# Optimization experiments

Hardware: AMD Instinct MI355X
Metric: run time of the kernel (lower is better)

Reference implementation:

```python
import jax, jax.numpy as jnp
import numpy as np

PC_RANGE = (-51.2, -51.2, -5.0, 51.2, 51.2, 3.0)
NUM_HEADS = 8
K_TOKENS = 512
DS = 4  # bev_downsample


def _ln(x, w, b):
    m = x.mean(-1, keepdims=True)
    v = ((x - m) ** 2).mean(-1, keepdims=True)
    return (x - m) * jax.lax.rsqrt(v + 1e-5) * w + b


def _mlp(x, w1, b1, w2, b2):
    return jnp.maximum(x @ w1.T + b1, 0.0) @ w2.T + b2


def setup_inputs() -> dict:
    key = jax.random.key(0)
    ks = jax.random.split(key, 16)
    B, N, Dq, Dkv, H, W = 2, 1220, 512, 256, 512, 512
    s = 0.02
    rn = lambda k, shp: jax.random.normal(k, shp, jnp.float32) * s
    inp = {
        'instance_feature': jax.random.normal(ks[0], (B, N, Dq), jnp.float32),
        'pts_feats': jax.random.normal(ks[1], (B, Dkv, H, W), jnp.float32),
        'anchor': jax.random.normal(ks[2], (B, N, 11), jnp.float32) * 20.0,
        # cross-attention (kdim=vdim=256, embed_dim=512)
        'qw': rn(ks[3], (Dq, Dq)), 'qb': jnp.zeros((Dq,), jnp.float32),
        'kw': rn(ks[4], (Dq, Dkv)), 'kb': jnp.zeros((Dq,), jnp.float32),
        'vw': rn(ks[5], (Dq, Dkv)), 'vb': jnp.zeros((Dq,), jnp.float32),
        'aow': rn(ks[6], (Dq, Dq)), 'aob': jnp.zeros((Dq,), jnp.float32),
        # layer norms
        'qn_w': jnp.ones((Dq,), jnp.float32), 'qn_b': jnp.zeros((Dq,), jnp.float32),
        'tn_w': jnp.ones((Dkv,), jnp.float32), 'tn_b': jnp.zeros((Dkv,), jnp.float32),
        'on_w': jnp.ones((Dq,), jnp.float32), 'on_b': jnp.zeros((Dq,), jnp.float32),
        # out_proj
        'opw': rn(ks[7], (Dq, Dq)), 'opb': jnp.zeros((Dq,), jnp.float32),
        # bev_pos_mlp: Linear(2,256) -> ReLU -> Linear(256,256)
        'bp_w1': rn(ks[8], (Dkv, 2)), 'bp_b1': jnp.zeros((Dkv,), jnp.float32),
        'bp_w2': rn(ks[9], (Dkv, Dkv)), 'bp_b2': jnp.zeros((Dkv,), jnp.float32),
        # anchor_pos_mlp: Linear(2,512) -> ReLU -> Linear(512,512)
        'ap_w1': rn(ks[10], (Dq, 2)), 'ap_b1': jnp.zeros((Dq,), jnp.float32),
        'ap_w2': rn(ks[11], (Dq, Dq)), 'ap_b2': jnp.zeros((Dq,), jnp.float32),
        # gate: Linear(512,512) -> ReLU -> Linear(512,512) -> Sigmoid, bias init -2.0
        'g_w1': rn(ks[12], (Dq, Dq)), 'g_b1': jnp.zeros((Dq,), jnp.float32),
        'g_w2': rn(ks[13], (Dq, Dq)), 'g_b2': jnp.full((Dq,), -2.0, jnp.float32),
    }
    return inp


def reference(instance_feature, pts_feats, anchor,
              qw, qb, kw, kb, vw, vb, aow, aob,
              qn_w, qn_b, tn_w, tn_b, on_w, on_b,
              opw, opb,
              bp_w1, bp_b1, bp_w2, bp_b2,
              ap_w1, ap_b1, ap_w2, ap_b2,
              g_w1, g_b1, g_w2, g_b2):
    B, C, H0, W0 = pts_feats.shape
    # avg_pool2d(kernel=stride=DS)
    H, W = H0 // DS, W0 // DS
    bev = pts_feats.reshape(B, C, H, DS, W, DS).mean(axis=(3, 5))  # [B,C,H,W]
    # topk token selection by mean squared activation
    score = (bev ** 2).mean(axis=1).reshape(B, H * W)
    K = min(K_TOKENS, H * W)
    _, idx = jax.lax.top_k(score, K)  # [B,K], sorted descending
    tokens = bev.reshape(B, C, H * W).transpose(0, 2, 1)  # [B,HW,C]
    lidar_tokens = jnp.take_along_axis(tokens, idx[..., None], axis=1)  # [B,K,C]
    ys = idx // W
    xs = idx % W
    token_pos = jnp.stack([(xs.astype(jnp.float32) + 0.5) / W,
                           (ys.astype(jnp.float32) + 0.5) / H], axis=-1)  # [B,K,2]
    lidar_tokens = lidar_tokens + _mlp(token_pos, bp_w1, bp_b1, bp_w2, bp_b2)
    # anchor positional prior (anchor detached in original)
    xr = (anchor[..., 0] - PC_RANGE[0]) / (PC_RANGE[3] - PC_RANGE[0])
    yr = (anchor[..., 1] - PC_RANGE[1]) / (PC_RANGE[4] - PC_RANGE[1])
    xy = jnp.clip(jnp.stack([xr, yr], axis=-1), 0.0, 1.0)
    query_input = instance_feature + _mlp(xy, ap_w1, ap_b1, ap_w2, ap_b2)
    query = _ln(query_input, qn_w, qn_b)
    kv = _ln(lidar_tokens, tn_w, tn_b)
    # multihead cross-attention (dropout off / eval mode)
    Dq = query.shape[-1]
    hd = Dq // NUM_HEADS
    q = (query @ qw.T + qb).reshape(B, -1, NUM_HEADS, hd)  # [B,N,h,d]
    k = (kv @ kw.T + kb).reshape(B, K, NUM_HEADS, hd)      # [B,K,h,d]
    v = (kv @ vw.T + vb).reshape(B, K, NUM_HEADS, hd)
    scale = 1.0 / jnp.sqrt(jnp.float32(hd))
    att = jax.nn.softmax(jnp.einsum('bnhd,bkhd->bhnk', q, k) * scale, axis=-1)
    ctx = jnp.einsum('bhnk,bkhd->bnhd', att, v).reshape(B, -1, Dq)
    ctx = ctx @ aow.T + aob  # MHA out_proj
    lidar_context = _ln(ctx @ opw.T + opb, on_w, on_b)
    gate = jax.nn.sigmoid(_mlp(query_input, g_w1, g_b1, g_w2, g_b2))
    return instance_feature + gate * lidar_context
```

## Files before the change

### kernel.cpp

```cpp
#include <hip/hip_runtime.h>
#include <hip/hip_bf16.h>
#include <math.h>

constexpr int BB  = 2;
constexpr int NN  = 1220;
constexpr int DKV = 256;
constexpr int H0  = 512, W0 = 512;
constexpr int HH  = 128, WW = 128;
constexpr int HW  = HH * WW;
constexpr int KT  = 512;
constexpr int MR  = BB * NN;

typedef __attribute__((ext_vector_type(8)))  short bf16x8;
typedef __attribute__((ext_vector_type(4)))  float f32x4;
typedef __attribute__((ext_vector_type(16))) float f32x16;

constexpr size_t B_BEV   = 0;
constexpr size_t B_SCORE = 33554432;
constexpr size_t B_IDX   = 33685504;
constexpr size_t B_WBF   = 33689600;
constexpr size_t B_KV    = 37359616;
constexpr size_t B_KG    = 37883904;
constexpr size_t B_VG    = 38932480;
constexpr size_t B_VT    = 39981056;
constexpr size_t B_H1    = 41029632;
constexpr size_t B_QI32  = 43651072;
constexpr size_t B_QI16  = 48893952;
constexpr size_t B_QUERY = 51515392;
constexpr size_t B_QG    = 54136832;
constexpr size_t B_CTX   = 56758272;
constexpr size_t B_AO    = 59379712;
constexpr size_t B_OPO   = 62001152;
constexpr size_t B_LC    = 67244032;
constexpr size_t B_G1    = 72486912;
constexpr size_t WS_NEED = 75112448;

constexpr size_t WO_QW = 0, WO_KW = 262144, WO_VW = 393216, WO_AOW = 524288,
                 WO_OPW = 786432, WO_APW2 = 1048576, WO_GW1 = 1310720, WO_GW2 = 1572864;

__device__ __forceinline__ void gload_lds16(void* lds, const void* g) {
  __builtin_amdgcn_global_load_lds((const __attribute__((address_space(1))) unsigned int*)g,
                                   (__attribute__((address_space(3))) unsigned int*)lds, 16, 0, 0);
}

__device__ __forceinline__ unsigned cvt_pk_bf16(float a, float b) {
  unsigned r;
  asm("v_cvt_pk_bf16_f32 %0, %1, %2" : "=v"(r) : "v"(a), "v"(b));
  return r;
}

__global__ __launch_bounds__(256) void wconv_kernel(
    const float* __restrict__ qw, const float* __restrict__ kw,
    const float* __restrict__ vw, const float* __restrict__ aow,
    const float* __restrict__ opw, const float* __restrict__ apw2,
    const float* __restrict__ gw1, const float* __restrict__ gw2,
    __hip_bfloat16* __restrict__ dst) {
  int i = blockIdx.x * 256 + threadIdx.x;
  const float* src; int off;
  if (i < 262144)       { src = qw;   off = 0; }
  else if (i < 393216)  { src = kw;   off = 262144; }
  else if (i < 524288)  { src = vw;   off = 393216; }
  else if (i < 786432)  { src = aow;  off = 524288; }
  else if (i < 1048576) { src = opw;  off = 786432; }
  else if (i < 1310720) { src = apw2; off = 1048576; }
  else if (i < 1572864) { src = gw1;  off = 1310720; }
  else                  { src = gw2;  off = 1572864; }
  dst[i] = __float2bfloat16(src[i - off]);
}

__global__ __launch_bounds__(256) void poolscore_kernel(const float* __restrict__ pts,
    float* __restrict__ bev, float* __restrict__ score) {
  int g = blockIdx.x * 256 + threadIdx.x;
  int b = g >> 14;
  int p = g & (HW - 1);
  int h = p >> 7, w = p & (WW - 1);
  const float* base = pts + (((size_t)(b * 256) * 512) + h * 4) * 512 + w * 4;
  float acc = 0.f;
#pragma unroll 4
  for (int c = 0; c < 256; ++c) {
    const float* pc = base + (size_t)c * 262144;
    float s = 0.f;
#pragma unroll
    for (int r = 0; r < 4; ++r) {
      float4 v = *(const float4*)(pc + r * W0);
      s += v.x + v.y + v.z + v.w;
    }
    float sv = s * (1.f / 16.f);
    bev[((size_t)(b * 256 + c) << 14) + p] = sv;
    acc += sv * sv;
  }
  score[g] = acc * (1.f / 256.f);
}

__global__ __launch_bounds__(1024) void topk_kernel(const float* __restrict__ score,
                                                    int* __restrict__ idx) {
  int b = blockIdx.x;
  const float* s = score + b * HW;
  __shared__ int hist[16][256];
  __shared__ int htot[256];
  __shared__ int pscan[1024];
  __shared__ int sh_digit, sh_need, sh_cnt;
  int tid = threadIdx.x;
  int wv = tid >> 6;
  unsigned prefix = 0;
  int need = KT;
  for (int pass = 0; pass < 4; ++pass) {
    int shift = 24 - pass * 8;
    if (tid < 256) {
#pragma unroll
      for (int w = 0; w < 16; ++w) hist[w][tid] = 0;
    }
    __syncthreads();
    for (int p = tid; p < HW; p += 1024) {
      unsigned u = __float_as_uint(s[p]);
      bool match = (pass == 0) || ((u >> (shift + 8)) == prefix);
      if (match) atomicAdd(&hist[wv][(u >> shift) & 255], 1);
    }
    __syncthreads();
    if (tid < 256) {
      int t = 0;
#pragma unroll
      for (int w = 0; w < 16; ++w) t += hist[w][tid];
      htot[tid] = t;
    }
    __syncthreads();
    for (int off = 1; off < 256; off <<= 1) {
      int v = 0;
      if (tid < 256) v = htot[tid] + ((tid + off < 256) ? htot[tid + off] : 0);
      __syncthreads();
      if (tid < 256) htot[tid] = v;
      __syncthreads();
    }
    if (tid < 256) {
      int sfx = htot[tid], sfx1 = (tid < 255) ? htot[tid + 1] : 0;
      if (sfx >= need && sfx1 < need) { sh_digit = tid; sh_need = need - sfx1; }
    }
    __syncthreads();
    prefix = (prefix << 8) | (unsigned)sh_digit;
    need = sh_need;
    __syncthreads();
  }
  unsigned T = prefix;
  int r = need;
  if (tid == 0) sh_cnt = 0;
  __syncthreads();
  for (int p = tid; p < HW; p += 1024) {
    if (__float_as_uint(s[p]) > T) {
      int pos = atomicAdd(&sh_cnt, 1);
      idx[b * KT + pos] = p;
    }
  }
  __syncthreads();
  int base = sh_cnt;
  int base0 = tid * 16;
  int cnt = 0;
#pragma unroll
  for (int j = 0; j < 16; ++j) cnt += (__float_as_uint(s[base0 + j]) == T);
  pscan[tid] = cnt;
  __syncthreads();
  for (int off = 1; off < 1024; off <<= 1) {
    int v = pscan[tid];
    int add = (tid >= off) ? pscan[tid - off] : 0;
    __syncthreads();
    pscan[tid] = v + add;
    __syncthreads();
  }
  int rank = pscan[tid] - cnt;
  for (int j = 0; j < 16 && rank < r; ++j) {
    int p = base0 + j;
    if (__float_as_uint(s[p]) == T) {
      idx[b * KT + base + rank] = p;
      ++rank;
    }
  }
}

__global__ __launch_bounds__(256) void token_kernel(const float* __restrict__ bev,
    const int* __restrict__ idx,
    const float* __restrict__ bw1, const float* __restrict__ bb1,
    const float* __restrict__ bw2, const float* __restrict__ bb2,
    const float* __restrict__ tw, const float* __restrict__ tb,
    __hip_bfloat16* __restrict__ kv) {
  int blk = blockIdx.x;
  int b = blk >> 9;
  int c = threadIdx.x;
  int p = idx[blk];
  float val = bev[((size_t)(b * DKV + c) << 14) + p];
  float px = ((p & (WW - 1)) + 0.5f) * (1.f / WW);
  float py = ((p >> 7) + 0.5f) * (1.f / HH);
  __shared__ float h1[DKV];
  __shared__ float red[DKV];
  h1[c] = fmaxf(bw1[c * 2] * px + bw1[c * 2 + 1] * py + bb1[c], 0.f);
  __syncthreads();
  float o = bb2[c];
  const float4* w4 = (const float4*)(bw2 + c * DKV);
#pragma unroll 4
  for (int j = 0; j < DKV / 4; ++j) {
    float4 w = w4[j];
    o += w.x * h1[j * 4] + w.y * h1[j * 4 + 1] + w.z * h1[j * 4 + 2] + w.w * h1[j * 4 + 3];
  }
  float tokv = val + o;
  red[c] = tokv; __syncthreads();
  for (int st = 128; st > 0; st >>= 1) { if (c < st) red[c] += red[c + st]; __syncthreads(); }
  float mean = red[0] * (1.f / DKV);
  __syncthreads();
  float d = tokv - mean;
  red[c] = d * d; __syncthreads();
  for (int st = 128; st > 0; st >>= 1) { if (c < st) red[c] += red[c + st]; __syncthreads(); }
  float inv = rsqrtf(red[0] * (1.f / DKV) + 1e-5f);
  kv[(size_t)blk * DKV + c] = __float2bfloat16(d * inv * tw[c] + tb[c]);
}

__global__ __launch_bounds__(256) void ap1_kernel(const float* __restrict__ anchor,
    const float* __restrict__ w1, const float* __restrict__ b1,
    __hip_bfloat16* __restrict__ h) {
  int g = blockIdx.x * 256 + threadIdx.x;
  int row = g >> 9, col = g & 511;
  float ax = anchor[row * 11 + 0];
  float ay = anchor[row * 11 + 1];
  float xr = fminf(fmaxf((ax + 51.2f) * (1.f / 102.4f), 0.f), 1.f);
  float yr = fminf(fmaxf((ay + 51.2f) * (1.f / 102.4f), 0.f), 1.f);
  h[g] = __float2bfloat16(fmaxf(w1[col * 2] * xr + w1[col * 2 + 1] * yr + b1[col], 0.f));
}

template <int EPI>
__global__ __launch_bounds__(256) void mgemm(
    const short* __restrict__ A, const short* __restrict__ W,
    const float* __restrict__ bias, const float* __restrict__ aux1,
    const float* __restrict__ aux2, void* __restrict__ o1, void* __restrict__ o2,
    int M, int Nd, int Kd) {
  __shared__ short As[2][64 * 64];
  __shared__ short Bs[2][64 * 64];
  const int tid = threadIdx.x;
  const int wave = tid >> 6, lane = tid & 63;
  const int m0 = blockIdx.y * 64, n0 = blockIdx.x * 64;
  const int wr = wave >> 1, wc = wave & 1;
  const int srow = lane >> 3, sslot = lane & 7;
  const int ss = sslot ^ srow;
  f32x4 acc[2][2];
#pragma unroll
  for (int i = 0; i < 2; ++i)
#pragma unroll
    for (int j = 0; j < 2; ++j) acc[i][j] = (f32x4){0.f, 0.f, 0.f, 0.f};

  const short* Abase = A + (size_t)(m0 + srow) * Kd + ss * 8;
  const short* Wbase = W + (size_t)(n0 + srow) * Kd + ss * 8;
  const int nk = Kd >> 6;

#define STAGE(buf, k0)                                                        \
  {                                                                           \
    _Pragma("unroll")                                                         \
    for (int u = 0; u < 2; ++u) {                                             \
      int unit = wave * 2 + u;                                                \
      gload_lds16(&As[buf][unit * 512], Abase + (size_t)(unit * 8) * Kd + (k0)); \
      gload_lds16(&Bs[buf][unit * 512], Wbase + (size_t)(unit * 8) * Kd + (k0)); \
    }                                                                         \
  }

  STAGE(0, 0);
  __syncthreads();
  for (int t = 0; t < nk; ++t) {
    if (t + 1 < nk) STAGE((t + 1) & 1, (t + 1) << 6);
    const short* as = As[t & 1];
    const short* bs = Bs[t & 1];
#pragma unroll
    for (int ks = 0; ks < 2; ++ks) {
      bf16x8 af[2], bf[2];
#pragma unroll
      for (int mf = 0; mf < 2; ++mf) {
        int rr = wr * 32 + mf * 16 + (lane & 15);
        int slot = (ks * 4 + (lane >> 4)) ^ (rr & 7);
        af[mf] = *(const bf16x8*)(as + rr * 64 + slot * 8);
      }
#pragma unroll
      for (int nf = 0; nf < 2; ++nf) {
        int rr = wc * 32 + nf * 16 + (lane & 15);
        int slot = (ks * 4 + (lane >> 4)) ^ (rr & 7);
        bf[nf] = *(const bf16x8*)(bs + rr * 64 + slot * 8);
      }
#pragma unroll
      for (int mf = 0; mf < 2; ++mf)
#pragma unroll
        for (int nf = 0; nf < 2; ++nf)
          acc[mf][nf] = __builtin_amdgcn_mfma_f32_16x16x32_bf16(af[mf], bf[nf], acc[mf][nf], 0, 0, 0);
    }
    __syncthreads();
  }
#undef STAGE
#pragma unroll
  for (int mf = 0; mf < 2; ++mf)
#pragma unroll
    for (int nf = 0; nf < 2; ++nf) {
      int col = n0 + wc * 32 + nf * 16 + (lane & 15);
      float bv = bias[col];
#pragma unroll
      for (int i = 0; i < 4; ++i) {
        int row = m0 + wr * 32 + mf * 16 + (lane >> 4) * 4 + i;
        if (row < M) {
          float v = acc[mf][nf][i] + bv;
          size_t off = (size_t)row * Nd + col;
          if (EPI == 0) ((__hip_bfloat16*)o1)[off] = __float2bfloat16(v);
          else if (EPI == 1) {
            v += aux1[off];
            ((float*)o1)[off] = v;
            ((__hip_bfloat16*)o2)[off] = __float2bfloat16(v);
          } else if (EPI == 2) ((__hip_bfloat16*)o1)[off] = __float2bfloat16(fmaxf(v, 0.f));
          else if (EPI == 3) ((__hip_bfloat16*)o1)[off] = __float2bfloat16(v * 0.125f);
          else if (EPI == 4) ((float*)o1)[off] = v;
          else if (EPI == 5) {
            float g = 1.f / (1.f + __expf(-v));
            ((float*)o1)[off] = aux1[off] + g * aux2[off];
          }
        }
      }
    }
}

template <int OUT_BF16>
__global__ __launch_bounds__(256) void ln512_kernel(const float* __restrict__ in,
    void* __restrict__ outp, const float* __restrict__ w, const float* __restrict__ bb) {
  int row = blockIdx.x, tid = threadIdx.x;
  float x0 = in[(size_t)row * 512 + tid];
  float x1 = in[(size_t)row * 512 + 256 + tid];
  __shared__ float rs[256], rq[256];
  rs[tid] = x0 + x1;
  rq[tid] = x0 * x0 + x1 * x1;
  __syncthreads();
  for (int o = 128; o > 0; o >>= 1) {
    if (tid < o) { rs[tid] += rs[tid + o]; rq[tid] += rq[tid + o]; }
    __syncthreads();
  }
  float mean = rs[0] * (1.f / 512.f);
  float var = rq[0] * (1.f / 512.f) - mean * mean;
  float inv = rsqrtf(var + 1e-5f);
  float y0 = (x0 - mean) * inv * w[tid] + bb[tid];
  float y1 = (x1 - mean) * inv * w[256 + tid] + bb[256 + tid];
  if (OUT_BF16) {
    ((__hip_bfloat16*)outp)[(size_t)row * 512 + tid] = __float2bfloat16(y0);
    ((__hip_bfloat16*)outp)[(size_t)row * 512 + 256 + tid] = __float2bfloat16(y1);
  } else {
    ((float*)outp)[(size_t)row * 512 + tid] = y0;
    ((float*)outp)[(size_t)row * 512 + 256 + tid] = y1;
  }
}

__global__ __launch_bounds__(256) void vtrans_kernel(const short* __restrict__ V,
                                                     short* __restrict__ Vt) {
  __shared__ short tile[128][72];
  int tc = blockIdx.x, h = blockIdx.y, b = blockIdx.z;
  int tid = threadIdx.x;
#pragma unroll
  for (int it = 0; it < 8; ++it) {
    int e = it * 256 + tid;
    int r = e >> 4, c = (e & 15) * 4;
    *(short4*)&tile[r][c] =
        *(const short4*)(V + ((size_t)(b * 512 + tc * 128 + r)) * 512 + h * 64 + c);
  }
  __syncthreads();
#pragma unroll
  for (int it = 0; it < 8; ++it) {
    int e = it * 256 + tid;
    int d = e >> 5, t4 = (e & 31) * 4;
    short4 v;
    v.x = tile[t4 + 0][d]; v.y = tile[t4 + 1][d];
    v.z = tile[t4 + 2][d]; v.w = tile[t4 + 3][d];
    *(short4*)(Vt + (((size_t)(b * 8 + h)) * 64 + d) * 512 + tc * 128 + t4) = v;
  }
}

__global__ __launch_bounds__(256) void attn_kernel(
    const short* __restrict__ Qg, const short* __restrict__ Kg,
    const short* __restrict__ Vt, __hip_bfloat16* __restrict__ ctx) {
  int tid = threadIdx.x;
  int wid = blockIdx.x * 4 + (tid >> 6);
  int lane = tid & 63;
  int l31 = lane & 31, lhi = lane >> 5;
  int qc = wid % 39;
  int bh = wid / 39;
  int h = bh & 7, b = bh >> 3;
  int n = qc * 32 + l31;
  size_t qrow = (size_t)b * NN + n;
  const short* qp = Qg + qrow * 512 + h * 64 + lhi * 8;
  bf16x8 qf0 = *(const bf16x8*)(qp);
  bf16x8 qf1 = *(const bf16x8*)(qp + 16);
  bf16x8 qf2 = *(const bf16x8*)(qp + 32);
  bf16x8 qf3 = *(const bf16x8*)(qp + 48);
  f32x16 ot0 = {}, ot1 = {};
  float m_run = -1e30f, lsum = 0.f;
  const short* kbase = Kg + ((size_t)(b * KT) + l31) * 512 + h * 64 + lhi * 8;
  const short* vbase = Vt + (((size_t)(b * 8 + h)) * 64 + l31) * 512 + lhi * 8;
  for (int tc = 0; tc < 16; ++tc) {
    const short* kp = kbase + (size_t)(tc * 32) * 512;
    bf16x8 kf0 = *(const bf16x8*)(kp);
    bf16x8 kf1 = *(const bf16x8*)(kp + 16);
    bf16x8 kf2 = *(const bf16x8*)(kp + 32);
    bf16x8 kf3 = *(const bf16x8*)(kp + 48);
    const short* vp = vbase + tc * 32;
    bf16x8 v00 = *(const bf16x8*)(vp);
    bf16x8 v01 = *(const bf16x8*)(vp + 16);
    bf16x8 v10 = *(const bf16x8*)(vp + 32 * 512);
    bf16x8 v11 = *(const bf16x8*)(vp + 32 * 512 + 16);
    f32x16 s = {};
    s = __builtin_amdgcn_mfma_f32_32x32x16_bf16(kf0, qf0, s, 0, 0, 0);
    s = __builtin_amdgcn_mfma_f32_32x32x16_bf16(kf1, qf1, s, 0, 0, 0);
    s = __builtin_amdgcn_mfma_f32_32x32x16_bf16(kf2, qf2, s, 0, 0, 0);
    s = __builtin_amdgcn_mfma_f32_32x32x16_bf16(kf3, qf3, s, 0, 0, 0);
    float pmax = s[0];
#pragma unroll
    for (int i = 1; i < 16; ++i) pmax = fmaxf(pmax, s[i]);
    pmax = fmaxf(pmax, __shfl_xor(pmax, 32));
    float m_new = fmaxf(m_run, pmax);
    float corr = __expf(m_run - m_new);
    m_run = m_new;
    lsum *= corr;
#pragma unroll
    for (int i = 0; i < 16; ++i) { ot0[i] *= corr; ot1[i] *= corr; }
    float p[16];
    float psum = 0.f;
#pragma unroll
    for (int i = 0; i < 16; ++i) { p[i] = __expf(s[i] - m_new); psum += p[i]; }
    lsum += psum;
    unsigned w0 = cvt_pk_bf16(p[0], p[1]),   w1 = cvt_pk_bf16(p[2], p[3]);
    unsigned w2 = cvt_pk_bf16(p[4], p[5]),   w3 = cvt_pk_bf16(p[6], p[7]);
    unsigned w4 = cvt_pk_bf16(p[8], p[9]),   w5 = cvt_pk_bf16(p[10], p[11]);
    unsigned w6 = cvt_pk_bf16(p[12], p[13]), w7 = cvt_pk_bf16(p[14], p[15]);
    unsigned sw0 = (unsigned)__shfl_xor((int)w0, 32), sw1 = (unsigned)__shfl_xor((int)w1, 32);
    unsigned sw2 = (unsigned)__shfl_xor((int)w2, 32), sw3 = (unsigned)__shfl_xor((int)w3, 32);
    unsigned sw4 = (unsigned)__shfl_xor((int)w4, 32), sw5 = (unsigned)__shfl_xor((int)w5, 32);
    unsigned sw6 = (unsigned)__shfl_xor((int)w6, 32), sw7 = (unsigned)__shfl_xor((int)w7, 32);
    union UU { unsigned u[4]; bf16x8 v; };
    UU ub0, ub1;
    ub0.u[0] = lhi ? sw2 : w0; ub0.u[1] = lhi ? sw3 : w1;
    ub0.u[2] = lhi ? w2 : sw0; ub0.u[3] = lhi ? w3 : sw1;
    ub1.u[0] = lhi ? sw6 : w4; ub1.u[1] = lhi ? sw7 : w5;
    ub1.u[2] = lhi ? w6 : sw4; ub1.u[3] = lhi ? w7 : sw5;
    ot0 = __builtin_amdgcn_mfma_f32_32x32x16_bf16(v00, ub0.v, ot0, 0, 0, 0);
    ot0 = __builtin_amdgcn_mfma_f32_32x32x16_bf16(v01, ub1.v, ot0, 0, 0, 0);
    ot1 = __builtin_amdgcn_mfma_f32_32x32x16_bf16(v10, ub0.v, ot1, 0, 0, 0);
    ot1 = __builtin_amdgcn_mfma_f32_32x32x16_bf16(v11, ub1.v, ot1, 0, 0, 0);
  }
  lsum += __shfl_xor(lsum, 32);
  float inv = 1.f / lsum;
  if (n < NN) {
    __hip_bfloat16* cp = ctx + qrow * 512 + h * 64;
#pragma unroll
    for (int r = 0; r < 16; ++r) {
      int d = (r & 3) + 8 * (r >> 2) + 4 * lhi;
      cp[d]      = __float2bfloat16(ot0[r] * inv);
      cp[32 + d] = __float2bfloat16(ot1[r] * inv);
    }
  }
}

extern "C" void kernel_launch(void* const* d_in, const int* in_sizes, int n_in,
                              void* d_out, int out_size, void* d_ws, size_t ws_size,
                              hipStream_t stream) {
  const float* inst   = (const float*)d_in[0];
  const float* pts    = (const float*)d_in[1];
  const float* anchor = (const float*)d_in[2];
  const float* qw  = (const float*)d_in[3];
  const float* qb  = (const float*)d_in[4];
  const float* kw  = (const float*)d_in[5];
  const float* kb  = (const float*)d_in[6];
  const float* vw  = (const float*)d_in[7];
  const float* vb  = (const float*)d_in[8];
  const float* aow = (const float*)d_in[9];
  const float* aob = (const float*)d_in[10];
  const float* qnw = (const float*)d_in[11];
  const float* qnb = (const float*)d_in[12];
  const float* tnw = (const float*)d_in[13];
  const float* tnb = (const float*)d_in[14];
  const float* onw = (const float*)d_in[15];
  const float* onb = (const float*)d_in[16];
  const float* opw = (const float*)d_in[17];
  const float* opb = (const float*)d_in[18];
  const float* bpw1 = (const float*)d_in[19];
  const float* bpb1 = (const float*)d_in[20];
  const float* bpw2 = (const float*)d_in[21];
  const float* bpb2 = (const float*)d_in[22];
  const float* apw1 = (const float*)d_in[23];
  const float* apb1 = (const float*)d_in[24];
  const float* apw2 = (const float*)d_in[25];
  const float* apb2 = (const float*)d_in[26];
  const float* gw1 = (const float*)d_in[27];
  const float* gb1 = (const float*)d_in[28];
  const float* gw2 = (const float*)d_in[29];
  const float* gb2 = (const float*)d_in[30];
  float* out = (float*)d_out;

  if (ws_size < WS_NEED) return;
  char* ws = (char*)d_ws;
  float* bev   = (float*)(ws + B_BEV);
  float* score = (float*)(ws + B_SCORE);
  int*   idx   = (int*)(ws + B_IDX);
  short* wbf   = (short*)(ws + B_WBF);
  __hip_bfloat16* kvb = (__hip_bfloat16*)(ws + B_KV);
  short* Kgb  = (short*)(ws + B_KG);
  short* Vgb  = (short*)(ws + B_VG);
  short* Vtb  = (short*)(ws + B_VT);
  short* h1b  = (short*)(ws + B_H1);
  float* qi32 = (float*)(ws + B_QI32);
  short* qi16 = (short*)(ws + B_QI16);
  short* qryb = (short*)(ws + B_QUERY);
  short* Qgb  = (short*)(ws + B_QG);
  short* ctxb = (short*)(ws + B_CTX);
  short* aobuf = (short*)(ws + B_AO);
  float* opo  = (float*)(ws + B_OPO);
  float* lc   = (float*)(ws + B_LC);
  short* g1b  = (short*)(ws + B_G1);

  wconv_kernel<<<7168, 256, 0, stream>>>(qw, kw, vw, aow, opw, apw2, gw1, gw2,
                                         (__hip_bfloat16*)wbf);
  poolscore_kernel<<<BB * HW / 256, 256, 0, stream>>>(pts, bev, score);
  topk_kernel<<<BB, 1024, 0, stream>>>(score, idx);
  token_kernel<<<BB * KT, 256, 0, stream>>>(bev, idx, bpw1, bpb1, bpw2, bpb2, tnw, tnb, kvb);
  mgemm<0><<<dim3(8, 16), 256, 0, stream>>>((const short*)kvb, wbf + WO_KW, kb,
                                            nullptr, nullptr, Kgb, nullptr, 1024, 512, 256);
  mgemm<0><<<dim3(8, 16), 256, 0, stream>>>((const short*)kvb, wbf + WO_VW, vb,
                                            nullptr, nullptr, Vgb, nullptr, 1024, 512, 256);
  vtrans_kernel<<<dim3(4, 8, BB), 256, 0, stream>>>(Vgb, Vtb);
  ap1_kernel<<<MR * 512 / 256, 256, 0, stream>>>(anchor, apw1, apb1, (__hip_bfloat16*)h1b);
  mgemm<1><<<dim3(8, 39), 256, 0, stream>>>(h1b, wbf + WO_APW2, apb2, inst, nullptr,
                                            qi32, qi16, MR, 512, 512);
  ln512_kernel<1><<<MR, 256, 0, stream>>>(qi32, qryb, qnw, qnb);
  mgemm<3><<<dim3(8, 39), 256, 0, stream>>>(qryb, wbf + WO_QW, qb, nullptr, nullptr,
                                            Qgb, nullptr, MR, 512, 512);
  attn_kernel<<<156, 256, 0, stream>>>(Qgb, Kgb, Vtb, (__hip_bfloat16*)ctxb);
  mgemm<0><<<dim3(8, 39), 256, 0, stream>>>(ctxb, wbf + WO_AOW, aob, nullptr, nullptr,
                                            aobuf, nullptr, MR, 512, 512);
  mgemm<4><<<dim3(8, 39), 256, 0, stream>>>(aobuf, wbf + WO_OPW, opb, nullptr, nullptr,
                                            opo, nullptr, MR, 512, 512);
  ln512_kernel<0><<<MR, 256, 0, stream>>>(opo, lc, onw, onb);
  mgemm<2><<<dim3(8, 39), 256, 0, stream>>>(qi16, wbf + WO_GW1, gb1, nullptr, nullptr,
                                            g1b, nullptr, MR, 512, 512);
  mgemm<5><<<dim3(8, 39), 256, 0, stream>>>(g1b, wbf + WO_GW2, gb2, inst, lc,
                                            out, nullptr, MR, 512, 512);
}
```

Baseline: 333.5 us.

## Fold attention out-proj into output projection and fuse K/V GEMMs with transpose

Precomputes a combined weight Wc = opw·aow and bias bc = opw·aob + opb, so the two back-to-back 512x512 projections on the attention context become one GEMM. The K and V projections now run as a single launch over blockIdx.z, and the V half writes directly in the transposed per-head layout, which removes the separate vtrans kernel and the Vg buffer. The anchor MLP first layer and the weight prep are merged into one prep kernel. The costs are an extra 512x512x512 weight-combine GEMM on every call and different bf16 rounding, because the combined weight is quantized once instead of the intermediate activation.

```diff
diff --git a/kernel.cpp b/kernel.cpp
--- a/kernel.cpp
+++ b/kernel.cpp
@@ -21,7 +21,7 @@
 constexpr size_t B_WBF   = 33689600;
 constexpr size_t B_KV    = 37359616;
 constexpr size_t B_KG    = 37883904;
-constexpr size_t B_VG    = 38932480;
+constexpr size_t B_AOWT  = 38932480;
 constexpr size_t B_VT    = 39981056;
 constexpr size_t B_H1    = 41029632;
 constexpr size_t B_QI32  = 43651072;
@@ -29,7 +29,8 @@
 constexpr size_t B_QUERY = 51515392;
 constexpr size_t B_QG    = 54136832;
 constexpr size_t B_CTX   = 56758272;
-constexpr size_t B_AO    = 59379712;
+constexpr size_t B_WC    = 59379712;
+constexpr size_t B_BC    = 60428288;
 constexpr size_t B_OPO   = 62001152;
 constexpr size_t B_LC    = 67244032;
 constexpr size_t B_G1    = 72486912;
@@ -49,23 +50,48 @@
   return r;
 }
 
-__global__ __launch_bounds__(256) void wconv_kernel(
+__global__ __launch_bounds__(256) void prep_kernel(
     const float* __restrict__ qw, const float* __restrict__ kw,
     const float* __restrict__ vw, const float* __restrict__ aow,
     const float* __restrict__ opw, const float* __restrict__ apw2,
     const float* __restrict__ gw1, const float* __restrict__ gw2,
-    __hip_bfloat16* __restrict__ dst) {
-  int i = blockIdx.x * 256 + threadIdx.x;
-  const float* src; int off;
-  if (i < 262144)       { src = qw;   off = 0; }
-  else if (i < 393216)  { src = kw;   off = 262144; }
-  else if (i < 524288)  { src = vw;   off = 393216; }
-  else if (i < 786432)  { src = aow;  off = 524288; }
-  else if (i < 1048576) { src = opw;  off = 786432; }
-  else if (i < 1310720) { src = apw2; off = 1048576; }
-  else if (i < 1572864) { src = gw1;  off = 1310720; }
-  else                  { src = gw2;  off = 1572864; }
-  dst[i] = __float2bfloat16(src[i - off]);
+    const float* __restrict__ anchor, const float* __restrict__ apw1,
+    const float* __restrict__ apb1, const float* __restrict__ aob,
+    const float* __restrict__ opb,
+    __hip_bfloat16* __restrict__ wbf, __hip_bfloat16* __restrict__ h1,
+    __hip_bfloat16* __restrict__ aowT, float* __restrict__ bc) {
+  int blk = blockIdx.x;
+  int tid = threadIdx.x;
+  if (blk < 7168) {
+    int i = blk * 256 + tid;
+    const float* src; int off;
+    if (i < 262144)       { src = qw;   off = 0; }
+    else if (i < 393216)  { src = kw;   off = 262144; }
+    else if (i < 524288)  { src = vw;   off = 393216; }
+    else if (i < 786432)  { src = aow;  off = 524288; }
+    else if (i < 1048576) { src = opw;  off = 786432; }
+    else if (i < 1310720) { src = apw2; off = 1048576; }
+    else if (i < 1572864) { src = gw1;  off = 1310720; }
+    else                  { src = gw2;  off = 1572864; }
+    wbf[i] = __float2bfloat16(src[i - off]);
+  } else if (blk < 12048) {
+    int g = (blk - 7168) * 256 + tid;
+    int row = g >> 9, col = g & 511;
+    float ax = anchor[row * 11 + 0];
+    float ay = anchor[row * 11 + 1];
+    float xr = fminf(fmaxf((ax + 51.2f) * (1.f / 102.4f), 0.f), 1.f);
+    float yr = fminf(fmaxf((ay + 51.2f) * (1.f / 102.4f), 0.f), 1.f);
+    h1[g] = __float2bfloat16(fmaxf(apw1[col * 2] * xr + apw1[col * 2 + 1] * yr + apb1[col], 0.f));
+  } else if (blk < 13072) {
+    int j = (blk - 12048) * 256 + tid;
+    int k = j >> 9, i2 = j & 511;
+    aowT[j] = __float2bfloat16(aow[i2 * 512 + k]);
+  } else {
+    int o = (blk - 13072) * 256 + tid;
+    float acc = opb[o];
+    for (int k = 0; k < 512; ++k) acc += opw[o * 512 + k] * aob[k];
+    bc[o] = acc;
+  }
 }
 
 __global__ __launch_bounds__(256) void poolscore_kernel(const float* __restrict__ pts,
@@ -211,18 +237,6 @@
   kv[(size_t)blk * DKV + c] = __float2bfloat16(d * inv * tw[c] + tb[c]);
 }
 
-__global__ __launch_bounds__(256) void ap1_kernel(const float* __restrict__ anchor,
-    const float* __restrict__ w1, const float* __restrict__ b1,
-    __hip_bfloat16* __restrict__ h) {
-  int g = blockIdx.x * 256 + threadIdx.x;
-  int row = g >> 9, col = g & 511;
-  float ax = anchor[row * 11 + 0];
-  float ay = anchor[row * 11 + 1];
-  float xr = fminf(fmaxf((ax + 51.2f) * (1.f / 102.4f), 0.f), 1.f);
-  float yr = fminf(fmaxf((ay + 51.2f) * (1.f / 102.4f), 0.f), 1.f);
-  h[g] = __float2bfloat16(fmaxf(w1[col * 2] * xr + w1[col * 2 + 1] * yr + b1[col], 0.f));
-}
-
 template <int EPI>
 __global__ __launch_bounds__(256) void mgemm(
     const short* __restrict__ A, const short* __restrict__ W,
@@ -237,6 +251,9 @@
   const int wr = wave >> 1, wc = wave & 1;
   const int srow = lane >> 3, sslot = lane & 7;
   const int ss = sslot ^ srow;
+  const short* Wp = W;
+  const float* biasp = bias;
+  if (EPI == 7 && blockIdx.z == 1) { Wp = (const short*)aux2; biasp = aux1; }
   f32x4 acc[2][2];
 #pragma unroll
   for (int i = 0; i < 2; ++i)
@@ -244,7 +261,7 @@
     for (int j = 0; j < 2; ++j) acc[i][j] = (f32x4){0.f, 0.f, 0.f, 0.f};
 
   const short* Abase = A + (size_t)(m0 + srow) * Kd + ss * 8;
-  const short* Wbase = W + (size_t)(n0 + srow) * Kd + ss * 8;
+  const short* Wbase = Wp + (size_t)(n0 + srow) * Kd + ss * 8;
   const int nk = Kd >> 6;
 
 #define STAGE(buf, k0)                                                        \
@@ -292,24 +309,38 @@
 #pragma unroll
     for (int nf = 0; nf < 2; ++nf) {
       int col = n0 + wc * 32 + nf * 16 + (lane & 15);
-      float bv = bias[col];
-#pragma unroll
-      for (int i = 0; i < 4; ++i) {
-        int row = m0 + wr * 32 + mf * 16 + (lane >> 4) * 4 + i;
-        if (row < M) {
-          float v = acc[mf][nf][i] + bv;
-          size_t off = (size_t)row * Nd + col;
-          if (EPI == 0) ((__hip_bfloat16*)o1)[off] = __float2bfloat16(v);
-          else if (EPI == 1) {
-            v += aux1[off];
-            ((float*)o1)[off] = v;
-            ((__hip_bfloat16*)o2)[off] = __float2bfloat16(v);
-          } else if (EPI == 2) ((__hip_bfloat16*)o1)[off] = __float2bfloat16(fmaxf(v, 0.f));
-          else if (EPI == 3) ((__hip_bfloat16*)o1)[off] = __float2bfloat16(v * 0.125f);
-          else if (EPI == 4) ((float*)o1)[off] = v;
-          else if (EPI == 5) {
-            float g = 1.f / (1.f + __expf(-v));
-            ((float*)o1)[off] = aux1[off] + g * aux2[off];
+      float bv = (EPI == 8) ? 0.f : biasp[col];
+      if (EPI == 7 && blockIdx.z == 1) {
+        int h = col >> 6, d = col & 63;
+        int row0 = m0 + wr * 32 + mf * 16 + (lane >> 4) * 4;
+        int bb2 = row0 >> 9, t0 = row0 & 511;
+        short4 sv;
+#pragma unroll
+        for (int i = 0; i < 4; ++i) {
+          __hip_bfloat16 x = __float2bfloat16(acc[mf][nf][i] + bv);
+          ((__hip_bfloat16*)&sv)[i] = x;
+        }
+        *(short4*)((short*)o2 + ((((size_t)(bb2 * 8 + h)) * 64 + d) << 9) + t0) = sv;
+      } else {
+#pragma unroll
+        for (int i = 0; i < 4; ++i) {
+          int row = m0 + wr * 32 + mf * 16 + (lane >> 4) * 4 + i;
+          if (row < M) {
+            float v = acc[mf][nf][i] + bv;
+            size_t off = (size_t)row * Nd + col;
+            if (EPI == 0 || EPI == 7 || EPI == 8)
+              ((__hip_bfloat16*)o1)[off] = __float2bfloat16(v);
+            else if (EPI == 1) {
+              v += aux1[off];
+              ((float*)o1)[off] = v;
+              ((__hip_bfloat16*)o2)[off] = __float2bfloat16(v);
+            } else if (EPI == 2) ((__hip_bfloat16*)o1)[off] = __float2bfloat16(fmaxf(v, 0.f));
+            else if (EPI == 3) ((__hip_bfloat16*)o1)[off] = __float2bfloat16(v * 0.125f);
+            else if (EPI == 4) ((float*)o1)[off] = v;
+            else if (EPI == 5) {
+              float g = 1.f / (1.f + __expf(-v));
+              ((float*)o1)[off] = aux1[off] + g * aux2[off];
+            }
           }
         }
       }
@@ -341,30 +372,6 @@
   } else {
     ((float*)outp)[(size_t)row * 512 + tid] = y0;
     ((float*)outp)[(size_t)row * 512 + 256 + tid] = y1;
-  }
-}
-
-__global__ __launch_bounds__(256) void vtrans_kernel(const short* __restrict__ V,
-                                                     short* __restrict__ Vt) {
-  __shared__ short tile[128][72];
-  int tc = blockIdx.x, h = blockIdx.y, b = blockIdx.z;
-  int tid = threadIdx.x;
-#pragma unroll
-  for (int it = 0; it < 8; ++it) {
-    int e = it * 256 + tid;
-    int r = e >> 4, c = (e & 15) * 4;
-    *(short4*)&tile[r][c] =
-        *(const short4*)(V + ((size_t)(b * 512 + tc * 128 + r)) * 512 + h * 64 + c);
-  }
-  __syncthreads();
-#pragma unroll
-  for (int it = 0; it < 8; ++it) {
-    int e = it * 256 + tid;
-    int d = e >> 5, t4 = (e & 31) * 4;
-    short4 v;
-    v.x = tile[t4 + 0][d]; v.y = tile[t4 + 1][d];
-    v.z = tile[t4 + 2][d]; v.w = tile[t4 + 3][d];
-    *(short4*)(Vt + (((size_t)(b * 8 + h)) * 64 + d) * 512 + tc * 128 + t4) = v;
   }
 }
 
@@ -496,7 +503,7 @@
   short* wbf   = (short*)(ws + B_WBF);
   __hip_bfloat16* kvb = (__hip_bfloat16*)(ws + B_KV);
   short* Kgb  = (short*)(ws + B_KG);
-  short* Vgb  = (short*)(ws + B_VG);
+  short* aowT = (short*)(ws + B_AOWT);
   short* Vtb  = (short*)(ws + B_VT);
   short* h1b  = (short*)(ws + B_H1);
   float* qi32 = (float*)(ws + B_QI32);
@@ -504,31 +511,31 @@
   short* qryb = (short*)(ws + B_QUERY);
   short* Qgb  = (short*)(ws + B_QG);
   short* ctxb = (short*)(ws + B_CTX);
-  short* aobuf = (short*)(ws + B_AO);
+  short* Wcb  = (short*)(ws + B_WC);
+  float* bcv  = (float*)(ws + B_BC);
   float* opo  = (float*)(ws + B_OPO);
   float* lc   = (float*)(ws + B_LC);
   short* g1b  = (short*)(ws + B_G1);
 
-  wconv_kernel<<<7168, 256, 0, stream>>>(qw, kw, vw, aow, opw, apw2, gw1, gw2,
-                                         (__hip_bfloat16*)wbf);
+  prep_kernel<<<13074, 256, 0, stream>>>(qw, kw, vw, aow, opw, apw2, gw1, gw2,
+                                         anchor, apw1, apb1, aob, opb,
+                                         (__hip_bfloat16*)wbf, (__hip_bfloat16*)h1b,
+                                         (__hip_bfloat16*)aowT, bcv);
+  mgemm<8><<<dim3(8, 8), 256, 0, stream>>>(wbf + WO_OPW, aowT, nullptr, nullptr,
+                                           nullptr, Wcb, nullptr, 512, 512, 512);
   poolscore_kernel<<<BB * HW / 256, 256, 0, stream>>>(pts, bev, score);
   topk_kernel<<<BB, 1024, 0, stream>>>(score, idx);
   token_kernel<<<BB * KT, 256, 0, stream>>>(bev, idx, bpw1, bpb1, bpw2, bpb2, tnw, tnb, kvb);
-  mgemm<0><<<dim3(8, 16), 256, 0, stream>>>((const short*)kvb, wbf + WO_KW, kb,
-                                            nullptr, nullptr, Kgb, nullptr, 1024, 512, 256);
-  mgemm<0><<<dim3(8, 16), 256, 0, stream>>>((const short*)kvb, wbf + WO_VW, vb,
-                                            nullptr, nullptr, Vgb, nullptr, 1024, 512, 256);
-  vtrans_kernel<<<dim3(4, 8, BB), 256, 0, stream>>>(Vgb, Vtb);
-  ap1_kernel<<<MR * 512 / 256, 256, 0, stream>>>(anchor, apw1, apb1, (__hip_bfloat16*)h1b);
+  mgemm<7><<<dim3(8, 16, 2), 256, 0, stream>>>((const short*)kvb, wbf + WO_KW, kb,
+                                               vb, (const float*)(wbf + WO_VW),
+                                               Kgb, Vtb, 1024, 512, 256);
   mgemm<1><<<dim3(8, 39), 256, 0, stream>>>(h1b, wbf + WO_APW2, apb2, inst, nullptr,
                                             qi32, qi16, MR, 512, 512);
   ln512_kernel<1><<<MR, 256, 0, stream>>>(qi32, qryb, qnw, qnb);
   mgemm<3><<<dim3(8, 39), 256, 0, stream>>>(qryb, wbf + WO_QW, qb, nullptr, nullptr,
                                             Qgb, nullptr, MR, 512, 512);
   attn_kernel<<<156, 256, 0, stream>>>(Qgb, Kgb, Vtb, (__hip_bfloat16*)ctxb);
-  mgemm<0><<<dim3(8, 39), 256, 0, stream>>>(ctxb, wbf + WO_AOW, aob, nullptr, nullptr,
-                                            aobuf, nullptr, MR, 512, 512);
-  mgemm<4><<<dim3(8, 39), 256, 0, stream>>>(aobuf, wbf + WO_OPW, opb, nullptr, nullptr,
+  mgemm<4><<<dim3(8, 39), 256, 0, stream>>>(ctxb, Wcb, bcv, nullptr, nullptr,
                                             opo, nullptr, MR, 512, 512);
   ln512_kernel<0><<<MR, 256, 0, stream>>>(opo, lc, onw, onb);
   mgemm<2><<<dim3(8, 39), 256, 0, stream>>>(qi16, wbf + WO_GW1, gb1, nullptr, nullptr,
```

After: 333.3 us. About the same (-0.1%).
